# Kernel optimization log

Hardware: AMD Instinct MI355X
Metric: run time of the kernel (lower is better)

Reference implementation:

```python
import jax, jax.numpy as jnp
import numpy as np

N = 8192  # number of DAG nodes


def setup_inputs() -> dict:
    key = jax.random.key(0)
    k1, k2, k3 = jax.random.split(key, 3)
    thresholds = jax.random.normal(k1, (N,), dtype=jnp.float32)
    # children in [-1, N): -1 marks a leaf (no child)
    left = jax.random.randint(k2, (N,), -1, N, dtype=jnp.int32)
    right = jax.random.randint(k3, (N,), -1, N, dtype=jnp.int32)
    return {"thresholds": thresholds, "left": left, "right": right}


def reference(thresholds, left, right):
    # BFS fixed-point reachability from node 0, N sequential relaxation steps.
    n_nodes = left.shape[0]

    def step(reachable, _):
        # route children of reachable non-leaf nodes into a scatter; dump
        # inactive slots into the sentinel index n_nodes (dropped on slice)
        active_left = jnp.where(reachable & (left >= 0), left, n_nodes)
        active_right = jnp.where(reachable & (right >= 0), right, n_nodes)
        new_reachable = jnp.zeros(n_nodes + 1, dtype=jnp.bool_)
        new_reachable = new_reachable.at[active_left].set(True)
        new_reachable = new_reachable.at[active_right].set(True)
        new_reachable = new_reachable.at[0].set(True)
        return (new_reachable[:n_nodes] | reachable, None)

    init = jnp.zeros(n_nodes, dtype=jnp.bool_).at[0].set(True)
    mask, _ = jax.lax.scan(step, init, None, length=n_nodes)
    return mask
```

## Files before the change

kernel.cpp:

```cpp
#include <hip/hip_runtime.h>


#define NMAX 8192
#define NW   (NMAX / 32)
#define BLK  256

__global__ __launch_bounds__(BLK) void dag_reach_kernel(
    const int* __restrict__ left,
    const int* __restrict__ right,
    int* __restrict__ out,
    int n)
{
    __shared__ int2         sLR[NMAX];
    __shared__ unsigned int reach[NW];
    __shared__ int          flag[2];

    const int tid = threadIdx.x;

    {
        const int4* l4 = (const int4*)left;
        const int4* r4 = (const int4*)right;
        const int nv = n / 4;
        for (int i = tid; i < nv; i += BLK) {
            int4 l = l4[i];
            int4 r = r4[i];
            int b = i * 4;
            sLR[b + 0] = make_int2(l.x, r.x);
            sLR[b + 1] = make_int2(l.y, r.y);
            sLR[b + 2] = make_int2(l.z, r.z);
            sLR[b + 3] = make_int2(l.w, r.w);
        }
    }
    reach[tid] = (tid == 0) ? 1u : 0u;
    if (tid < 2) flag[tid] = 0;
    __syncthreads();

    unsigned int expd = 0u;
    const int base = tid * 32;
    volatile unsigned int* vreach = (volatile unsigned int*)reach;

    for (int pass = 0; ; ++pass) {
        bool changed = false;

        for (;;) {
            unsigned int pend = vreach[tid] & ~expd;
            if (!pend) break;
            changed = true;
            expd |= pend;
            do {
                int b = __ffs(pend) - 1;
                pend &= pend - 1;
                int2 lr = sLR[base + b];
                if (lr.x >= 0) atomicOr(&reach[lr.x >> 5], 1u << (lr.x & 31));
                if (lr.y >= 0) atomicOr(&reach[lr.y >> 5], 1u << (lr.y & 31));
            } while (pend);
        }

        if (changed)  flag[pass & 1] = 1;
        if (tid == 0) flag[(pass + 1) & 1] = 0;
        __syncthreads();
        int f = flag[pass & 1];
        __syncthreads();
        if (!f) break;
    }

    {
        int4* o4 = (int4*)out;
        const int nv = n / 4;
        for (int i = tid; i < nv; i += BLK) {
            unsigned int w = reach[i >> 3];
            int sh = (i & 7) * 4;
            int4 v;
            v.x = (int)((w >> (sh + 0)) & 1u);
            v.y = (int)((w >> (sh + 1)) & 1u);
            v.z = (int)((w >> (sh + 2)) & 1u);
            v.w = (int)((w >> (sh + 3)) & 1u);
            o4[i] = v;
        }
    }
}

extern "C" void kernel_launch(void* const* d_in, const int* in_sizes, int n_in,
                              void* d_out, int out_size, void* d_ws, size_t ws_size,
                              hipStream_t stream)
{
    const int* left  = (const int*)d_in[1];
    const int* right = (const int*)d_in[2];
    int* out = (int*)d_out;
    const int n = in_sizes[1];

    dag_reach_kernel<<<1, BLK, 0, stream>>>(left, right, out, n);
}
```

Before: 84.09 us.

## Run reachability in a single wavefront with ballot-based convergence

Shrinks the block from 256 threads to one 64-lane wavefront, where each lane owns four reach words (128 nodes). The shared flag array and the double-barrier termination check are replaced by a wave-wide __any vote on pending bits. This removes cross-wavefront barriers and flag traffic per pass, at the cost of fewer threads for the global loads and more serial bit expansion per lane.

Result: slower. 102.7 us (+22.2%).

```diff
diff --git a/kernel.cpp b/kernel.cpp
--- a/kernel.cpp
+++ b/kernel.cpp
@@ -2,8 +2,7 @@
 
 
 #define NMAX 8192
-#define NW   (NMAX / 32)
-#define BLK  256
+#define BLK  64
 
 __global__ __launch_bounds__(BLK) void dag_reach_kernel(
     const int* __restrict__ left,
@@ -11,17 +10,16 @@
     int* __restrict__ out,
     int n)
 {
-    __shared__ int2         sLR[NMAX];
-    __shared__ unsigned int reach[NW];
-    __shared__ int          flag[2];
+    __shared__ int2 sLR[NMAX];
+    __shared__ __align__(16) unsigned int reach[NMAX / 32];
 
-    const int tid = threadIdx.x;
+    const int lane = threadIdx.x;
 
     {
         const int4* l4 = (const int4*)left;
         const int4* r4 = (const int4*)right;
         const int nv = n / 4;
-        for (int i = tid; i < nv; i += BLK) {
+        for (int i = lane; i < nv; i += BLK) {
             int4 l = l4[i];
             int4 r = r4[i];
             int b = i * 4;
@@ -31,51 +29,50 @@
             sLR[b + 3] = make_int2(l.w, r.w);
         }
     }
-    reach[tid] = (tid == 0) ? 1u : 0u;
-    if (tid < 2) flag[tid] = 0;
+    {
+        uint4 z = make_uint4(lane == 0 ? 1u : 0u, 0u, 0u, 0u);
+        ((uint4*)reach)[lane] = z;
+    }
     __syncthreads();
 
-    unsigned int expd = 0u;
-    const int base = tid * 32;
-    volatile unsigned int* vreach = (volatile unsigned int*)reach;
+    unsigned int expd0 = 0u, expd1 = 0u, expd2 = 0u, expd3 = 0u;
+    const int nbase = lane * 128;
 
-    for (int pass = 0; ; ++pass) {
-        bool changed = false;
+    for (;;) {
+        uint4 w = ((const uint4*)reach)[lane];
+        unsigned int p0 = w.x & ~expd0;
+        unsigned int p1 = w.y & ~expd1;
+        unsigned int p2 = w.z & ~expd2;
+        unsigned int p3 = w.w & ~expd3;
+        if (!__any((p0 | p1 | p2 | p3) != 0u)) break;
+        expd0 |= p0; expd1 |= p1; expd2 |= p2; expd3 |= p3;
 
-        for (;;) {
-            unsigned int pend = vreach[tid] & ~expd;
-            if (!pend) break;
-            changed = true;
-            expd |= pend;
-            do {
+        unsigned int pw[4] = {p0, p1, p2, p3};
+        #pragma unroll
+        for (int wi = 0; wi < 4; ++wi) {
+            unsigned int pend = pw[wi];
+            const int wb = nbase + wi * 32;
+            while (pend) {
                 int b = __ffs(pend) - 1;
                 pend &= pend - 1;
-                int2 lr = sLR[base + b];
+                int2 lr = sLR[wb + b];
                 if (lr.x >= 0) atomicOr(&reach[lr.x >> 5], 1u << (lr.x & 31));
                 if (lr.y >= 0) atomicOr(&reach[lr.y >> 5], 1u << (lr.y & 31));
-            } while (pend);
+            }
         }
-
-        if (changed)  flag[pass & 1] = 1;
-        if (tid == 0) flag[(pass + 1) & 1] = 0;
         __syncthreads();
-        int f = flag[pass & 1];
-        __syncthreads();
-        if (!f) break;
     }
 
     {
         int4* o4 = (int4*)out;
         const int nv = n / 4;
-        for (int i = tid; i < nv; i += BLK) {
+        for (int i = lane; i < nv; i += BLK) {
             unsigned int w = reach[i >> 3];
             int sh = (i & 7) * 4;
-            int4 v;
-            v.x = (int)((w >> (sh + 0)) & 1u);
-            v.y = (int)((w >> (sh + 1)) & 1u);
-            v.z = (int)((w >> (sh + 2)) & 1u);
-            v.w = (int)((w >> (sh + 3)) & 1u);
-            o4[i] = v;
+            o4[i] = make_int4((int)((w >> (sh + 0)) & 1u),
+                              (int)((w >> (sh + 1)) & 1u),
+                              (int)((w >> (sh + 2)) & 1u),
+                              (int)((w >> (sh + 3)) & 1u));
         }
     }
 }
```
